# Kernel tuning notes

Measured on AMD Instinct MI355X. Metric: run time of the kernel, lower is better.

Reference implementation:

```python
import jax, jax.numpy as jnp
import numpy as np

NUM_USERS = 200_000
NUM_ITEMS = 100_000
N = NUM_USERS + NUM_ITEMS
D = 32
E = 9_600_000
N_LAYERS = 3


def setup_inputs() -> dict:
    key = jax.random.key(0)
    k1, k2, k3, k4, k5 = jax.random.split(key, 5)
    rows = jax.random.randint(k1, (E,), 0, N, dtype=jnp.int32)
    cols = jax.random.randint(k2, (E,), 0, N, dtype=jnp.int32)
    # normalized-adjacency-like positive values
    vals = jax.random.uniform(k3, (E,), dtype=jnp.float32) * 0.05
    # xavier-uniform-ish embedding init
    bound = float(np.sqrt(6.0 / (NUM_USERS + D)))
    user_w = jax.random.uniform(k4, (NUM_USERS, D), dtype=jnp.float32,
                                minval=-bound, maxval=bound)
    bound_i = float(np.sqrt(6.0 / (NUM_ITEMS + D)))
    item_w = jax.random.uniform(k5, (NUM_ITEMS, D), dtype=jnp.float32,
                                minval=-bound_i, maxval=bound_i)
    return {"rows": rows, "cols": cols, "vals": vals,
            "user_w": user_w, "item_w": item_w}


def _spmm(rows, cols, vals, x):
    # A_hat @ x for COO A_hat: gather source features, scale, scatter-add to rows.
    msgs = vals[:, None] * x[cols]                 # [E, D]
    return jax.ops.segment_sum(msgs, rows, num_segments=N)  # [N, D]


def reference(rows, cols, vals, user_w, item_w):
    x0 = jnp.concatenate([user_w, item_w], axis=0)  # [N, D]
    x = x0
    acc = x0
    for _ in range(N_LAYERS):
        x = _spmm(rows, cols, vals, x)
        acc = acc + x
    x_mean = acc / (N_LAYERS + 1)                   # mean over layer stack
    users = x_mean[:NUM_USERS]
    items = x_mean[NUM_USERS:]
    return (users, items)
```

## Files before the change

kernel.cpp:

```cpp
#include <hip/hip_runtime.h>
#include <hip/hip_fp16.h>
#include <stdint.h>

#define NUM_USERS 200000
#define NUM_ITEMS 100000
#define NN (NUM_USERS + NUM_ITEMS)
#define D 32
#define NE 9600000
#define TOTAL (NN * D)

#define RPB2 128
#define B2 ((NN + RPB2 - 1) / RPB2)
#define CAP 5120

#define TPB_A 1024
#define EPT 16
#define EPB_A (TPB_A * EPT)

#define TPB_H 1024
#define EPT_H 32
#define EPB_H (TPB_H * EPT_H)
#define NB_H ((NE + EPB_H - 1) / EPB_H)

__global__ __launch_bounds__(256) void init_x_acc(
    const float4* __restrict__ user_w, const float4* __restrict__ item_w,
    ushort4* __restrict__ xh, float4* __restrict__ acc) {
    int i = blockIdx.x * 256 + threadIdx.x;
    const int total4 = TOTAL / 4;
    const int ub4 = (NUM_USERS * D) / 4;
    if (i < total4) {
        float4 v = (i < ub4) ? user_w[i] : item_w[i - ub4];
        acc[i] = v;
        ushort4 h;
        h.x = __half_as_ushort(__float2half(v.x));
        h.y = __half_as_ushort(__float2half(v.y));
        h.z = __half_as_ushort(__float2half(v.z));
        h.w = __half_as_ushort(__float2half(v.w));
        xh[i] = h;
    }
}

__global__ __launch_bounds__(TPB_H) void bucket_hist(
    const int4* __restrict__ rows4, int* __restrict__ bcounts) {
    __shared__ int hist[B2];
    int tid = threadIdx.x;
    for (int i = tid; i < B2; i += TPB_H) hist[i] = 0;
    __syncthreads();
    int base4 = blockIdx.x * (EPB_H / 4);
    #pragma unroll
    for (int k = 0; k < EPT_H / 4; ++k) {
        int i4 = base4 + k * TPB_H + tid;
        if (i4 < NE / 4) {
            int4 r = rows4[i4];
            atomicAdd(&hist[r.x >> 7], 1);
            atomicAdd(&hist[r.y >> 7], 1);
            atomicAdd(&hist[r.z >> 7], 1);
            atomicAdd(&hist[r.w >> 7], 1);
        }
    }
    __syncthreads();
    for (int b = tid; b < B2; b += TPB_H) {
        int c = hist[b];
        if (c) atomicAdd(&bcounts[b], c);
    }
}

__global__ __launch_bounds__(1024) void scan_buckets(
    const int* __restrict__ bcounts, int* __restrict__ bstart,
    int* __restrict__ bfill) {
    __shared__ int lds[1024];
    int t = threadIdx.x;
    int v[4];
    int s = 0;
    #pragma unroll
    for (int k = 0; k < 4; ++k) {
        int b = t * 4 + k;
        v[k] = (b < B2) ? bcounts[b] : 0;
        s += v[k];
    }
    lds[t] = s;
    __syncthreads();
    for (int off = 1; off < 1024; off <<= 1) {
        int u = (t >= off) ? lds[t - off] : 0;
        __syncthreads();
        lds[t] += u;
        __syncthreads();
    }
    int ex = lds[t] - s;
    #pragma unroll
    for (int k = 0; k < 4; ++k) {
        int b = t * 4 + k;
        if (b < B2) { bstart[b] = ex; bfill[b] = ex; }
        ex += v[k];
    }
    if (t == 1023) bstart[B2] = ex;
}

__global__ __launch_bounds__(TPB_A) void partition_edges(
    const int4* __restrict__ rows4, const int4* __restrict__ cols4,
    const float4* __restrict__ vals4, int* __restrict__ bfill,
    int2* __restrict__ temp) {
    __shared__ int hist[B2];
    int tid = threadIdx.x;
    for (int i = tid; i < B2; i += TPB_A) hist[i] = 0;
    __syncthreads();

    int base4 = blockIdx.x * (EPB_A / 4);
    uint32_t brank[EPT];

    #pragma unroll
    for (int k = 0; k < EPT / 4; ++k) {
        int i4 = base4 + k * TPB_A + tid;
        if (i4 < NE / 4) {
            int4 r = rows4[i4];
            uint32_t b0 = (uint32_t)r.x >> 7, b1 = (uint32_t)r.y >> 7;
            uint32_t b2 = (uint32_t)r.z >> 7, b3 = (uint32_t)r.w >> 7;
            brank[k * 4 + 0] = (b0 << 20) | (uint32_t)((r.x & 127) << 13) | (uint32_t)atomicAdd(&hist[b0], 1);
            brank[k * 4 + 1] = (b1 << 20) | (uint32_t)((r.y & 127) << 13) | (uint32_t)atomicAdd(&hist[b1], 1);
            brank[k * 4 + 2] = (b2 << 20) | (uint32_t)((r.z & 127) << 13) | (uint32_t)atomicAdd(&hist[b2], 1);
            brank[k * 4 + 3] = (b3 << 20) | (uint32_t)((r.w & 127) << 13) | (uint32_t)atomicAdd(&hist[b3], 1);
        }
    }
    __syncthreads();
    for (int b = tid; b < B2; b += TPB_A) {
        int c = hist[b];
        if (c) hist[b] = atomicAdd(&bfill[b], c);
    }
    __syncthreads();

    #pragma unroll
    for (int k = 0; k < EPT / 4; ++k) {
        int i4 = base4 + k * TPB_A + tid;
        if (i4 < NE / 4) {
            int4 c = cols4[i4];
            float4 v = vals4[i4];
            uint32_t br; int pos; int2 cv;
            br = brank[k * 4 + 0]; pos = hist[br >> 20] + (int)(br & 0x1FFFu);
            cv.x = (int)(((br >> 13) & 127u) << 19) | c.x; cv.y = __float_as_int(v.x); temp[pos] = cv;
            br = brank[k * 4 + 1]; pos = hist[br >> 20] + (int)(br & 0x1FFFu);
            cv.x = (int)(((br >> 13) & 127u) << 19) | c.y; cv.y = __float_as_int(v.y); temp[pos] = cv;
            br = brank[k * 4 + 2]; pos = hist[br >> 20] + (int)(br & 0x1FFFu);
            cv.x = (int)(((br >> 13) & 127u) << 19) | c.z; cv.y = __float_as_int(v.z); temp[pos] = cv;
            br = brank[k * 4 + 3]; pos = hist[br >> 20] + (int)(br & 0x1FFFu);
            cv.x = (int)(((br >> 13) & 127u) << 19) | c.w; cv.y = __float_as_int(v.w); temp[pos] = cv;
        }
    }
}

__global__ __launch_bounds__(256) void sort_bucket2(
    const int* __restrict__ bstart, const int2* __restrict__ temp,
    int* __restrict__ row_start, int2* __restrict__ colval) {
    __shared__ int2 stage[CAP];
    __shared__ int lstart[RPB2];
    __shared__ int lfill[RPB2];
    int b = blockIdx.x;
    int row0 = b * RPB2;
    int rcount = NN - row0; if (rcount > RPB2) rcount = RPB2;
    int tid = threadIdx.x;
    int s = bstart[b];
    int count = bstart[b + 1] - s;

    if (tid < RPB2) lfill[tid] = 0;
    __syncthreads();

    for (int i = tid; i < count; i += 256) {
        int rl = temp[s + i].x >> 19;
        atomicAdd(&lfill[rl], 1);
    }
    __syncthreads();

    int val = (tid < RPB2) ? lfill[tid] : 0;
    if (tid < RPB2) lstart[tid] = val;
    __syncthreads();
    for (int off = 1; off < RPB2; off <<= 1) {
        int u = (tid >= off && tid < RPB2) ? lstart[tid - off] : 0;
        __syncthreads();
        if (tid < RPB2) lstart[tid] += u;
        __syncthreads();
    }
    int ex = (tid < RPB2) ? lstart[tid] - val : 0;
    if (tid < RPB2) {
        lstart[tid] = ex;
        lfill[tid] = 0;
        if (tid < rcount) row_start[row0 + tid] = s + ex;
    }
    if (b == 0 && tid == 0) row_start[NN] = NE;
    __syncthreads();

    if (count <= CAP) {
        for (int i = tid; i < count; i += 256) {
            int2 e = temp[s + i];
            int rl = e.x >> 19;
            int pos = lstart[rl] + atomicAdd(&lfill[rl], 1);
            stage[pos] = make_int2(e.x & 0x7FFFF, e.y);
        }
        __syncthreads();
        for (int i = tid; i < count; i += 256) colval[s + i] = stage[i];
    } else {
        for (int i = tid; i < count; i += 256) {
            int2 e = temp[s + i];
            int rl = e.x >> 19;
            int pos = lstart[rl] + atomicAdd(&lfill[rl], 1);
            colval[s + pos] = make_int2(e.x & 0x7FFFF, e.y);
        }
    }
}

template <bool LAST>
__global__ __launch_bounds__(256) void spmm_csr(
    const int* __restrict__ row_start, const int2* __restrict__ colval,
    const __half* __restrict__ xh, __half* __restrict__ yh,
    float* __restrict__ acc) {
    int lane = threadIdx.x & 31;
    int row = blockIdx.x * 8 + (threadIdx.x >> 5);
    if (row >= NN) return;
    int s = row_start[row];
    int e = row_start[row + 1];
    float s0 = 0.f, s1 = 0.f, s2 = 0.f, s3 = 0.f;
    float s4 = 0.f, s5 = 0.f, s6 = 0.f, s7 = 0.f;
    int i = s;
    for (; i + 7 < e; i += 8) {
        int2 a0 = colval[i];
        int2 a1 = colval[i + 1];
        int2 a2 = colval[i + 2];
        int2 a3 = colval[i + 3];
        int2 a4 = colval[i + 4];
        int2 a5 = colval[i + 5];
        int2 a6 = colval[i + 6];
        int2 a7 = colval[i + 7];
        s0 += __int_as_float(a0.y) * __half2float(xh[a0.x * D + lane]);
        s1 += __int_as_float(a1.y) * __half2float(xh[a1.x * D + lane]);
        s2 += __int_as_float(a2.y) * __half2float(xh[a2.x * D + lane]);
        s3 += __int_as_float(a3.y) * __half2float(xh[a3.x * D + lane]);
        s4 += __int_as_float(a4.y) * __half2float(xh[a4.x * D + lane]);
        s5 += __int_as_float(a5.y) * __half2float(xh[a5.x * D + lane]);
        s6 += __int_as_float(a6.y) * __half2float(xh[a6.x * D + lane]);
        s7 += __int_as_float(a7.y) * __half2float(xh[a7.x * D + lane]);
    }
    for (; i < e; ++i) {
        int2 a = colval[i];
        s0 += __int_as_float(a.y) * __half2float(xh[a.x * D + lane]);
    }
    float sum = ((s0 + s1) + (s2 + s3)) + ((s4 + s5) + (s6 + s7));
    int idx = row * D + lane;
    if (!LAST) yh[idx] = __float2half(sum);
    float a = acc[idx] + sum;
    acc[idx] = LAST ? a * 0.25f : a;
}

extern "C" void kernel_launch(void* const* d_in, const int* in_sizes, int n_in,
                              void* d_out, int out_size, void* d_ws, size_t ws_size,
                              hipStream_t stream) {
    const int*   rows   = (const int*)d_in[0];
    const int*   cols   = (const int*)d_in[1];
    const float* vals   = (const float*)d_in[2];
    const float* user_w = (const float*)d_in[3];
    const float* item_w = (const float*)d_in[4];

    float* acc = (float*)d_out;

    __half* xh = (__half*)d_ws;
    __half* yh = xh + (size_t)TOTAL;
    int2*  temp = (int2*)d_ws;
    int2*  colval = (int2*)((char*)d_ws + 2ull * (size_t)TOTAL * sizeof(float));
    int*   bcounts = (int*)(colval + (size_t)NE);
    int*   bstart = bcounts + B2;
    int*   bfill = bstart + (B2 + 1);
    int*   row_start = bfill + B2;

    const int vec_blocks   = (TOTAL / 4 + 255) / 256;
    const int partA_blocks = (NE + EPB_A - 1) / EPB_A;
    const int row_blocks   = (NN + 7) / 8;

    hipMemsetAsync(bcounts, 0, (size_t)B2 * sizeof(int), stream);
    bucket_hist<<<NB_H, TPB_H, 0, stream>>>((const int4*)rows, bcounts);
    scan_buckets<<<1, 1024, 0, stream>>>(bcounts, bstart, bfill);
    partition_edges<<<partA_blocks, TPB_A, 0, stream>>>(
        (const int4*)rows, (const int4*)cols, (const float4*)vals, bfill, temp);
    sort_bucket2<<<B2, 256, 0, stream>>>(bstart, temp, row_start, colval);

    init_x_acc<<<vec_blocks, 256, 0, stream>>>(
        (const float4*)user_w, (const float4*)item_w, (ushort4*)xh, (float4*)acc);

    spmm_csr<false><<<row_blocks, 256, 0, stream>>>(row_start, colval, xh, yh, acc);
    spmm_csr<false><<<row_blocks, 256, 0, stream>>>(row_start, colval, yh, xh, acc);
    spmm_csr<true ><<<row_blocks, 256, 0, stream>>>(row_start, colval, xh, yh, acc);
}
```

Before: 932.2 us.

## Remap SpMM to one wavefront per row with 8 edges in parallel

The CSR SpMM kernel now assigns a full 64-lane wavefront per row. Eight lane groups each handle a different edge and load 4 half features as one 8-byte vector, then partial sums are combined with cross-lane shuffles. Previously a 32-lane group walked edges serially with scalar half loads. The aim is more parallel gathers in flight and fewer load instructions. The cost is shuffle reductions, a padded tail, and only 8 lanes doing the output writes.

After: 868.8 us. -6.8%, faster.

```diff
diff --git a/kernel.cpp b/kernel.cpp
--- a/kernel.cpp
+++ b/kernel.cpp
@@ -211,41 +211,79 @@
     const int* __restrict__ row_start, const int2* __restrict__ colval,
     const __half* __restrict__ xh, __half* __restrict__ yh,
     float* __restrict__ acc) {
-    int lane = threadIdx.x & 31;
-    int row = blockIdx.x * 8 + (threadIdx.x >> 5);
+    int lane = threadIdx.x & 63;
+    int grp = lane >> 3;
+    int fq = lane & 7;
+    int row = (blockIdx.x * 256 + threadIdx.x) >> 6;
     if (row >= NN) return;
     int s = row_start[row];
     int e = row_start[row + 1];
-    float s0 = 0.f, s1 = 0.f, s2 = 0.f, s3 = 0.f;
-    float s4 = 0.f, s5 = 0.f, s6 = 0.f, s7 = 0.f;
+    if (s == e) {
+        if (lane < 8) {
+            size_t idx = (size_t)row * D + lane * 4;
+            if (!LAST) *(uint2*)(yh + idx) = make_uint2(0u, 0u);
+            float4 av = *(const float4*)(acc + idx);
+            if (LAST) { av.x *= 0.25f; av.y *= 0.25f; av.z *= 0.25f; av.w *= 0.25f; }
+            *(float4*)(acc + idx) = av;
+        }
+        return;
+    }
+    float a0 = 0.f, a1 = 0.f, a2 = 0.f, a3 = 0.f;
+    float b0 = 0.f, b1 = 0.f, b2 = 0.f, b3 = 0.f;
     int i = s;
-    for (; i + 7 < e; i += 8) {
-        int2 a0 = colval[i];
-        int2 a1 = colval[i + 1];
-        int2 a2 = colval[i + 2];
-        int2 a3 = colval[i + 3];
-        int2 a4 = colval[i + 4];
-        int2 a5 = colval[i + 5];
-        int2 a6 = colval[i + 6];
-        int2 a7 = colval[i + 7];
-        s0 += __int_as_float(a0.y) * __half2float(xh[a0.x * D + lane]);
-        s1 += __int_as_float(a1.y) * __half2float(xh[a1.x * D + lane]);
-        s2 += __int_as_float(a2.y) * __half2float(xh[a2.x * D + lane]);
-        s3 += __int_as_float(a3.y) * __half2float(xh[a3.x * D + lane]);
-        s4 += __int_as_float(a4.y) * __half2float(xh[a4.x * D + lane]);
-        s5 += __int_as_float(a5.y) * __half2float(xh[a5.x * D + lane]);
-        s6 += __int_as_float(a6.y) * __half2float(xh[a6.x * D + lane]);
-        s7 += __int_as_float(a7.y) * __half2float(xh[a7.x * D + lane]);
-    }
-    for (; i < e; ++i) {
-        int2 a = colval[i];
-        s0 += __int_as_float(a.y) * __half2float(xh[a.x * D + lane]);
-    }
-    float sum = ((s0 + s1) + (s2 + s3)) + ((s4 + s5) + (s6 + s7));
-    int idx = row * D + lane;
-    if (!LAST) yh[idx] = __float2half(sum);
-    float a = acc[idx] + sum;
-    acc[idx] = LAST ? a * 0.25f : a;
+    for (; i + 16 <= e; i += 16) {
+        int2 cvA = colval[i + grp];
+        int2 cvB = colval[i + 8 + grp];
+        uint2 hA = *(const uint2*)(xh + (size_t)cvA.x * D + fq * 4);
+        uint2 hB = *(const uint2*)(xh + (size_t)cvB.x * D + fq * 4);
+        float vA = __int_as_float(cvA.y);
+        float vB = __int_as_float(cvB.y);
+        float2 fA0 = __half22float2(*(__half2*)&hA.x);
+        float2 fA1 = __half22float2(*(__half2*)&hA.y);
+        float2 fB0 = __half22float2(*(__half2*)&hB.x);
+        float2 fB1 = __half22float2(*(__half2*)&hB.y);
+        a0 += vA * fA0.x; a1 += vA * fA0.y; a2 += vA * fA1.x; a3 += vA * fA1.y;
+        b0 += vB * fB0.x; b1 += vB * fB0.y; b2 += vB * fB1.x; b3 += vB * fB1.y;
+    }
+    if (i < e) {
+        int iA = i + grp;
+        int iB = i + 8 + grp;
+        int cA = (iA < e) ? iA : (e - 1);
+        int cB = (iB < e) ? iB : (e - 1);
+        int2 cvA = colval[cA];
+        int2 cvB = colval[cB];
+        uint2 hA = *(const uint2*)(xh + (size_t)cvA.x * D + fq * 4);
+        uint2 hB = *(const uint2*)(xh + (size_t)cvB.x * D + fq * 4);
+        float vA = (iA < e) ? __int_as_float(cvA.y) : 0.f;
+        float vB = (iB < e) ? __int_as_float(cvB.y) : 0.f;
+        float2 fA0 = __half22float2(*(__half2*)&hA.x);
+        float2 fA1 = __half22float2(*(__half2*)&hA.y);
+        float2 fB0 = __half22float2(*(__half2*)&hB.x);
+        float2 fB1 = __half22float2(*(__half2*)&hB.y);
+        a0 += vA * fA0.x; a1 += vA * fA0.y; a2 += vA * fA1.x; a3 += vA * fA1.y;
+        b0 += vB * fB0.x; b1 += vB * fB0.y; b2 += vB * fB1.x; b3 += vB * fB1.y;
+    }
+    a0 += b0; a1 += b1; a2 += b2; a3 += b3;
+    #pragma unroll
+    for (int m = 8; m <= 32; m <<= 1) {
+        a0 += __shfl_xor(a0, m, 64);
+        a1 += __shfl_xor(a1, m, 64);
+        a2 += __shfl_xor(a2, m, 64);
+        a3 += __shfl_xor(a3, m, 64);
+    }
+    if (lane < 8) {
+        size_t idx = (size_t)row * D + lane * 4;
+        if (!LAST) {
+            __half2 h01 = __float22half2_rn(make_float2(a0, a1));
+            __half2 h23 = __float22half2_rn(make_float2(a2, a3));
+            *(uint2*)(yh + idx) =
+                make_uint2(*(uint32_t*)&h01, *(uint32_t*)&h23);
+        }
+        float4 av = *(const float4*)(acc + idx);
+        av.x += a0; av.y += a1; av.z += a2; av.w += a3;
+        if (LAST) { av.x *= 0.25f; av.y *= 0.25f; av.z *= 0.25f; av.w *= 0.25f; }
+        *(float4*)(acc + idx) = av;
+    }
 }
 
 extern "C" void kernel_launch(void* const* d_in, const int* in_sizes, int n_in,
@@ -270,7 +308,7 @@
 
     const int vec_blocks   = (TOTAL / 4 + 255) / 256;
     const int partA_blocks = (NE + EPB_A - 1) / EPB_A;
-    const int row_blocks   = (NN + 7) / 8;
+    const int row_blocks   = (NN + 3) / 4;
 
     hipMemsetAsync(bcounts, 0, (size_t)B2 * sizeof(int), stream);
     bucket_hist<<<NB_H, TPB_H, 0, stream>>>((const int4*)rows, bcounts);
```
